# Optimization experiments

Hardware: AMD Instinct MI355X
Metric: run time of the kernel (lower is better)

Reference implementation:

```python
import jax, jax.numpy as jnp
import numpy as np

B, C_IN, H, W = 2, 256, 48, 48
OC, G, KH, KW, PH, PW = 256, 4, 7, 7, 3, 3


def _patches(y, Hn, Wn):
    # y: (B, C, Hp, Wp) -> (B, C, KH, KW, Hn, Wn); stride=1, dilation=1
    return jnp.stack([
        jnp.stack([y[:, :, i:i + Hn, j:j + Wn] for j in range(KW)], axis=2)
        for i in range(KH)
    ], axis=2)


def setup_inputs() -> dict:
    key = jax.random.key(0)
    k1, k2, k3, k4 = jax.random.split(key, 4)
    fan_out = 3 * OC  # 1x1 conv, kaiming fan_out
    conv_w = jax.random.normal(k2, (3 * OC, C_IN), dtype=jnp.float32) * np.sqrt(2.0 / fan_out).astype(np.float32)
    return {
        "x": jax.random.normal(k1, (B, C_IN, H, W), dtype=jnp.float32),
        "conv_w": conv_w,
        "rpe_h": jax.random.normal(k3, (G, 1, KH, 1, (OC // G) // 2), dtype=jnp.float32),
        "rpe_w": jax.random.normal(k4, (G, 1, 1, KW, (OC // G) // 2), dtype=jnp.float32),
    }


def reference(x, conv_w, rpe_h, rpe_w):
    b, c, h, w = x.shape
    goc = OC // G
    c2 = goc // 2
    K = KH * KW
    center = (K - 1) // 2
    ci, cj = center // KW, center % KW

    # 1x1 conv to 3*OC channels, then zero-pad (equiv. to Conv2d(padding) + bias=False)
    y = jnp.einsum('bchw,oc->bohw', x, conv_w)
    y = jnp.pad(y, ((0, 0), (0, 0), (PH, PH), (PW, PW)))
    Hn = h + 2 * PH - (KH - 1)
    Wn = w + 2 * PW - (KW - 1)
    P = Hn * Wn

    q_full, k_full, v_full = jnp.split(y, 3, axis=1)

    # query: only the center element of each window is used
    query = q_full[:, :, ci:ci + Hn, cj:cj + Wn].reshape(b, G, goc, P)
    query = jnp.transpose(query, (0, 1, 3, 2))  # (B,G,P,goc)

    # key: full windows + relative position embeddings
    kp = _patches(k_full, Hn, Wn).reshape(b, G, goc, KH, KW, P)
    key = jnp.transpose(kp, (0, 1, 5, 3, 4, 2))  # (B,G,P,KH,KW,goc)
    key = jnp.concatenate((key[..., :c2] + rpe_h, key[..., c2:] + rpe_w), axis=1)  # (B,2G,P,KH,KW,c2)
    key = key.reshape(b, G, P, K, goc)  # row-major reshape matches torch

    vp = _patches(v_full, Hn, Wn).reshape(b, G, goc, K, P)
    value = jnp.transpose(vp, (0, 1, 4, 3, 2))  # (B,G,P,K,goc)

    att = jax.nn.softmax(jnp.einsum('bgpc,bgpkc->bgpk', query, key), axis=-1)
    out = jnp.einsum('bgpk,bgpkc->bgpc', att, value)  # (B,G,P,goc)
    out = jnp.transpose(out, (0, 1, 3, 2)).reshape(b, OC, Hn, Wn)
    return out
```

## Files before the change

kernel.cpp:

```cpp
#include <hip/hip_runtime.h>

#define BB   2
#define CIN  256
#define OC3  768
#define NG   4
#define GOC  64
#define C2   32
#define KK   49
#define PP   2304
#define HALF_P 1152

#define RS      56
#define BROWS   54
#define BSTRIDE (BROWS * RS * OC3)
#define IOFF    ((3 * RS + 3) * OC3)

#define Y2_BYTES  (BB * BROWS * RS * OC3 * 4)
#define XT_OFF    Y2_BYTES
#define WT_OFF    (XT_OFF + BB * PP * 512 * 2)

typedef __attribute__((ext_vector_type(8))) short bf16x8;
typedef __attribute__((ext_vector_type(4))) float f32x4;

static __device__ __forceinline__ unsigned short f2bf_rne(float x) {
    unsigned int u = __float_as_uint(x);
    unsigned int r = u + 0x7FFFu + ((u >> 16) & 1u);
    return (unsigned short)(r >> 16);
}
static __device__ __forceinline__ float bf2f(unsigned short h) {
    return __uint_as_float(((unsigned int)h) << 16);
}

static __device__ __forceinline__ void gll16(const short* g, short* l) {
    __builtin_amdgcn_global_load_lds(
        (const __attribute__((address_space(1))) unsigned int*)g,
        (__attribute__((address_space(3))) unsigned int*)l,
        16, 0, 0);
}

template <int C>
static __device__ __forceinline__ float dppf(float x) {
    return __int_as_float(__builtin_amdgcn_update_dpp(
        0, __float_as_int(x), C, 0xF, 0xF, true));
}
template <int D>
static __device__ __forceinline__ float xor_lane(float x) {
    if constexpr (D == 1)       return dppf<0xB1>(x);
    else if constexpr (D == 2)  return dppf<0x4E>(x);
    else if constexpr (D == 4)  return dppf<0x141>(dppf<0x4E>(dppf<0xB1>(x)));
    else if constexpr (D == 8)  return dppf<0x128>(x);
    else                        return __shfl_xor(x, D, 64);
}
template <int N> struct IC { static constexpr int value = N; };

#define ROW4  (RS * OC3 / 4)
#define REG1  (6 * ROW4)
#define COLS4 (OC3 / 4)

__global__ __launch_bounds__(256) void prep(
    float* __restrict__ Y2,
    const float* __restrict__ W, short* __restrict__ Wt,
    const float* __restrict__ X, short* __restrict__ Xt)
{
    __shared__ float tile[64][65];
    const int bid = blockIdx.x;
    const int t   = threadIdx.x;

    if (bid < 1080) {
        const int idx = (bid % 540) * 256 + t;
        const int b   = bid / 540;
        float4* Yb = (float4*)(Y2 + (size_t)b * BSTRIDE);
        const float4 z = make_float4(0.f, 0.f, 0.f, 0.f);
        if (idx < REG1) {
            int r6  = idx / ROW4;
            int rem = idx - r6 * ROW4;
            int r   = (r6 < 3) ? r6 : 48 + r6;
            Yb[r * ROW4 + rem] = z;
        } else {
            int i2  = idx - REG1;
            int r   = 3 + i2 / (8 * COLS4);
            int rem = i2 - (r - 3) * (8 * COLS4);
            int cg  = rem / COLS4;
            int c   = (cg < 3) ? cg : 48 + cg;
            int ch4 = rem - cg * COLS4;
            Yb[(r * RS + c) * COLS4 + ch4] = z;
        }
    } else if (bid < 1848) {
        int tt = (bid - 1080) * 256 + t;
        int o = tt >> 8, c = tt & 255;
        float v = W[tt];
        unsigned short hi = f2bf_rne(v);
        unsigned short lo = f2bf_rne(v - bf2f(hi));
        Wt[(size_t)o * 512 + c]       = (short)hi;
        Wt[(size_t)o * 512 + 256 + c] = (short)lo;
    } else {
        const int blk = bid - 1848;
        const int p0  = (blk % 36) * 64;
        const int c0  = ((blk / 36) & 3) * 64;
        const int b   = blk / 144;

        const float* Xb = X + (size_t)b * CIN * PP;
        #pragma unroll
        for (int r = 0; r < 16; ++r) {
            int idx = r * 256 + t;
            int c = idx >> 6, p = idx & 63;
            tile[c][p] = Xb[(size_t)(c0 + c) * PP + p0 + p];
        }
        __syncthreads();
        short* Xo = Xt + (size_t)b * PP * 512;
        #pragma unroll
        for (int r = 0; r < 16; ++r) {
            int idx = r * 256 + t;
            int p = idx >> 6, c = idx & 63;
            float v = tile[c][p];
            unsigned short hi = f2bf_rne(v);
            unsigned short lo = f2bf_rne(v - bf2f(hi));
            size_t base = (size_t)(p0 + p) * 512 + c0 + c;
            Xo[base]       = (short)hi;
            Xo[base + 256] = (short)lo;
        }
    }
}

__global__ __launch_bounds__(256, 4) void conv_mfma(
    const short* __restrict__ Wt,
    const short* __restrict__ Xt,
    float* __restrict__ Y2)
{
    __shared__ short As[64 * 32];
    __shared__ short Bs[64 * 32];

    const int tid = threadIdx.x;
    const int bn  = blockIdx.x;
    const int bm  = blockIdx.y;
    const int b   = blockIdx.z;
    const int om0 = bm * 64, pn0 = bn * 64;

    const int lane = tid & 63, w = tid >> 6;
    const int oq = (w & 1) * 32, pq = (w >> 1) * 32;
    const int ln15 = lane & 15, q = lane >> 4;

    const int R  = (w << 4) + (lane >> 2);
    const int sd = (lane & 3) ^ ((R >> 1) & 3);
    const short* gAq = Wt + (size_t)(om0 + R) * 512 + sd * 8;
    const short* gBq = Xt + (size_t)b * PP * 512 + (size_t)(pn0 + R) * 512 + sd * 8;
    short* ldsA = As + w * 512;
    short* ldsB = Bs + w * 512;

    const int swz = q ^ ((ln15 >> 1) & 3);

    f32x4 acc[2][2] = {};

    for (int k0 = 0; k0 < 768; k0 += 32) {
        const int wk = (k0 < 256) ? k0 : k0 - 256;
        const int xk = (k0 < 512) ? k0 : k0 - 512;
        __syncthreads();
        gll16(gAq + wk, ldsA);
        gll16(gBq + xk, ldsB);
        __syncthreads();

        bf16x8 af[2], bf[2];
        #pragma unroll
        for (int i = 0; i < 2; ++i) {
            af[i] = *(const bf16x8*)&As[(oq + i * 16 + ln15) * 32 + swz * 8];
            bf[i] = *(const bf16x8*)&Bs[(pq + i * 16 + ln15) * 32 + swz * 8];
        }
        #pragma unroll
        for (int i = 0; i < 2; ++i)
            #pragma unroll
            for (int j = 0; j < 2; ++j)
                acc[i][j] = __builtin_amdgcn_mfma_f32_16x16x32_bf16(
                    af[i], bf[j], acc[i][j], 0, 0, 0);
    }

    float* Yb = Y2 + (size_t)b * BSTRIDE + IOFF;
    #pragma unroll
    for (int i = 0; i < 2; ++i) {
        #pragma unroll
        for (int j = 0; j < 2; ++j) {
            int o = om0 + oq + i * 16 + q * 4;
            int p = pn0 + pq + j * 16 + ln15;
            int h = p / 48, ww = p - h * 48;
            *(f32x4*)&Yb[(size_t)(h * RS + ww) * OC3 + o] = acc[i][j];
        }
    }
}

struct TagH { static constexpr bool value = true;  };
struct TagW { static constexpr bool value = false; };

__global__ __launch_bounds__(256, 6) void attn_kernel(
    const float* __restrict__ Y2,
    const float* __restrict__ rpe_h,
    const float* __restrict__ rpe_w,
    float* __restrict__ out)
{
    __shared__ float xpose[4][65];

    const int tid  = threadIdx.x;
    const int lane = tid & 63;
    const int w    = tid >> 6;
    const int bx     = blockIdx.x;
    const int wblock = (bx & 7) * 576 + (bx >> 3);
    const int wid    = wblock * 4 + w;
    const int pq   = wid % PP;
    const int g    = (wid / PP) & (NG - 1);
    const int b    = wid / (PP * NG);
    const int ph   = pq / 48;
    const int pw   = pq - ph * 48;

    const float* Yb = Y2 + (size_t)b * BSTRIDE + IOFF;

    const float qv = Yb[(size_t)(ph * RS + pw) * OC3 + g * GOC + lane];

    const int t   = (pq >= HALF_P) ? 1 : 0;
    const int qpr = pq - t * HALF_P;
    const int p0  = 2 * qpr;
    const int ph0 = p0 / 48;
    const int pw0 = p0 - ph0 * 48;
    const int g2  = 2 * g + t;
    const bool use_h = (g2 < NG);
    const int  kch   = use_h ? (CIN + g2 * GOC) : (CIN + (g2 - NG) * GOC + C2);
    const float* rb  = use_h ? (rpe_h + g2 * 7 * C2) : (rpe_w + (g2 - NG) * 7 * C2);

    const int  c  = lane & 31;
    const bool hi = (lane >= 32);

    const float R0 = rb[0 * C2 + c], R1 = rb[1 * C2 + c], R2 = rb[2 * C2 + c],
                R3 = rb[3 * C2 + c], R4 = rb[4 * C2 + c], R5 = rb[5 * C2 + c],
                R6 = rb[6 * C2 + c];

    const float* kb = Yb + (size_t)(ph0 * RS + pw0) * OC3 + kch + c;

    auto rget = [&](int idx) -> float {
        return idx == 0 ? R0 : idx == 1 ? R1 : idx == 2 ? R2 :
               idx == 3 ? R3 : idx == 4 ? R4 : idx == 5 ? R5 : R6;
    };

    auto tree = [&](auto tag) -> float {
        constexpr bool UH = decltype(tag)::value;
        auto chunkprod = [&](int l) -> float {
            int m0 = 2 * l,     h10 = (m0 >= KK), k0 = m0 - KK * h10;
            int m1 = 2 * l + 1, h11 = (m1 >= KK), k1 = m1 - KK * h11;
            int i0 = k0 / 7, j0 = k0 % 7, i1 = k1 / 7, j1 = k1 % 7;
            int d0 = ((i0 - 3) * RS + (h10 + j0 - 3)) * OC3;
            int d1 = ((i1 - 3) * RS + (h11 + j1 - 3)) * OC3;
            float kv = kb[hi ? d1 : d0];
            float ra = UH ? rget(i0) : rget(j0);
            float rc = UH ? rget(i1) : rget(j1);
            kv += hi ? rc : ra;
            return qv * kv;
        };
        auto val = [&](int jj) -> float {
            if (2 * jj >= KK) return 0.f;
            float pa = chunkprod(2 * jj);
            float pb = (2 * jj + 1 < KK) ? chunkprod(2 * jj + 1) : 0.f;
            float u  = (lane & 1) ? pb : pa;
            float ww = (lane & 1) ? pa : pb;
            return u + xor_lane<1>(ww);
        };
        auto comb = [&](auto dc, float x, float y) -> float {
            constexpr int d = decltype(dc)::value;
            float u  = (lane & d) ? y : x;
            float ww = (lane & d) ? x : y;
            return u + xor_lane<d>(ww);
        };
        float acc32[2];
        #pragma unroll
        for (int a = 0; a < 2; ++a) {
            float acc16[2];
            #pragma unroll
            for (int bq = 0; bq < 2; ++bq) {
                float acc8[2];
                #pragma unroll
                for (int cq2 = 0; cq2 < 2; ++cq2) {
                    float acc4t[2];
                    #pragma unroll
                    for (int dq = 0; dq < 2; ++dq) {
                        float acc2[2];
                        #pragma unroll
                        for (int eq = 0; eq < 2; ++eq)
                            acc2[eq] = val(a * 16 + bq * 8 + cq2 * 4 + dq * 2 + eq);
                        acc4t[dq] = comb(IC<2>{}, acc2[0], acc2[1]);
                    }
                    acc8[cq2] = comb(IC<4>{}, acc4t[0], acc4t[1]);
                }
                acc16[bq] = comb(IC<8>{}, acc8[0], acc8[1]);
            }
            acc32[a] = comb(IC<16>{}, acc16[0], acc16[1]);
        }
        return comb(IC<32>{}, acc32[0], acc32[1]);
    };

    const float logit = use_h ? tree(TagH{}) : tree(TagW{});

    float mx = logit;
    mx = fmaxf(mx, xor_lane<1>(mx));
    mx = fmaxf(mx, xor_lane<2>(mx));
    mx = fmaxf(mx, xor_lane<4>(mx));
    mx = fmaxf(mx, xor_lane<8>(mx));
    mx = fmaxf(mx, xor_lane<16>(mx));
    mx = fmaxf(mx, xor_lane<32>(mx));
    float e = (lane < KK) ? __expf(logit - mx) : 0.f;
    float ssum = e;
    ssum += xor_lane<1>(ssum);
    ssum += xor_lane<2>(ssum);
    ssum += xor_lane<4>(ssum);
    ssum += xor_lane<8>(ssum);
    ssum += xor_lane<16>(ssum);
    ssum += xor_lane<32>(ssum);
    const float att = e / ssum;

    float acc = 0.f;
    const float* vb = Yb + (size_t)(ph * RS + pw) * OC3 + 2 * CIN + g * GOC + lane;
    #pragma unroll
    for (int k = 0; k < KK; ++k) {
        int i = k / 7, j = k % 7;
        int doff = ((i - 3) * RS + (j - 3)) * OC3;
        float ak = __uint_as_float(
            __builtin_amdgcn_readlane(__float_as_uint(att), k));
        acc = fmaf(ak, vb[doff], acc);
    }

    xpose[w][lane] = acc;
    __syncthreads();
    const int wid0 = wblock * 4;
    const int pq0  = wid0 % PP;
    const int g0   = (wid0 / PP) & (NG - 1);
    const int b0   = wid0 / (PP * NG);
    const int ch   = tid >> 2;
    const int w2   = tid & 3;
    out[((size_t)b0 * 256 + g0 * GOC + ch) * PP + pq0 + w2] = xpose[w2][ch];
}

extern "C" void kernel_launch(void* const* d_in, const int* in_sizes, int n_in,
                              void* d_out, int out_size, void* d_ws, size_t ws_size,
                              hipStream_t stream)
{
    const float* x  = (const float*)d_in[0];
    const float* w  = (const float*)d_in[1];
    const float* rh = (const float*)d_in[2];
    const float* rw = (const float*)d_in[3];

    float* Y2 = (float*)d_ws;
    short* Xt = (short*)((char*)d_ws + XT_OFF);
    short* Wt = (short*)((char*)d_ws + WT_OFF);

    prep<<<2136, 256, 0, stream>>>(Y2, w, Wt, x, Xt);
    conv_mfma<<<dim3(36, 12, BB), 256, 0, stream>>>(Wt, Xt, Y2);
    attn_kernel<<<(BB * NG * PP) / 4, 256, 0, stream>>>(Y2, rh, rw, (float*)d_out);
}
```

Baseline: 110.6 us.

## Double-buffer conv LDS loads and move Y2 border zeroing into conv kernel

The conv GEMM loop now uses two LDS buffers, so the global-to-LDS load for the next K step is issued before the current step's MFMAs, and one barrier per iteration is dropped. The zero-padding of the Y2 border is moved out of the prep kernel into extra blocks of the conv grid (bm >= 12). This shortens prep and lets the zeroing run alongside the GEMM blocks. LDS use per block doubles, which may affect occupancy, and the extra grid rows add some scheduling overhead.

```diff
diff --git a/kernel.cpp b/kernel.cpp
--- a/kernel.cpp
+++ b/kernel.cpp
@@ -58,7 +58,6 @@
 #define COLS4 (OC3 / 4)
 
 __global__ __launch_bounds__(256) void prep(
-    float* __restrict__ Y2,
     const float* __restrict__ W, short* __restrict__ Wt,
     const float* __restrict__ X, short* __restrict__ Xt)
 {
@@ -66,9 +65,58 @@
     const int bid = blockIdx.x;
     const int t   = threadIdx.x;
 
-    if (bid < 1080) {
-        const int idx = (bid % 540) * 256 + t;
-        const int b   = bid / 540;
+    if (bid < 768) {
+        int tt = bid * 256 + t;
+        int o = tt >> 8, c = tt & 255;
+        float v = W[tt];
+        unsigned short hi = f2bf_rne(v);
+        unsigned short lo = f2bf_rne(v - bf2f(hi));
+        Wt[(size_t)o * 512 + c]       = (short)hi;
+        Wt[(size_t)o * 512 + 256 + c] = (short)lo;
+    } else {
+        const int blk = bid - 768;
+        const int p0  = (blk % 36) * 64;
+        const int c0  = ((blk / 36) & 3) * 64;
+        const int b   = blk / 144;
+
+        const float* Xb = X + (size_t)b * CIN * PP;
+        #pragma unroll
+        for (int r = 0; r < 16; ++r) {
+            int idx = r * 256 + t;
+            int c = idx >> 6, p = idx & 63;
+            tile[c][p] = Xb[(size_t)(c0 + c) * PP + p0 + p];
+        }
+        __syncthreads();
+        short* Xo = Xt + (size_t)b * PP * 512;
+        #pragma unroll
+        for (int r = 0; r < 16; ++r) {
+            int idx = r * 256 + t;
+            int p = idx >> 6, c = idx & 63;
+            float v = tile[c][p];
+            unsigned short hi = f2bf_rne(v);
+            unsigned short lo = f2bf_rne(v - bf2f(hi));
+            size_t base = (size_t)(p0 + p) * 512 + c0 + c;
+            Xo[base]       = (short)hi;
+            Xo[base + 256] = (short)lo;
+        }
+    }
+}
+
+__global__ __launch_bounds__(256, 4) void conv_mfma(
+    const short* __restrict__ Wt,
+    const short* __restrict__ Xt,
+    float* __restrict__ Y2)
+{
+    __shared__ short As[2][64 * 32];
+    __shared__ short Bs[2][64 * 32];
+
+    const int tid = threadIdx.x;
+    const int bn  = blockIdx.x;
+    const int bm  = blockIdx.y;
+    const int b   = blockIdx.z;
+
+    if (bm >= 12) {
+        const int idx = ((bm - 12) * 36 + bn) * 256 + tid;
         float4* Yb = (float4*)(Y2 + (size_t)b * BSTRIDE);
         const float4 z = make_float4(0.f, 0.f, 0.f, 0.f);
         if (idx < REG1) {
@@ -85,55 +133,9 @@
             int ch4 = rem - cg * COLS4;
             Yb[(r * RS + c) * COLS4 + ch4] = z;
         }
-    } else if (bid < 1848) {
-        int tt = (bid - 1080) * 256 + t;
-        int o = tt >> 8, c = tt & 255;
-        float v = W[tt];
-        unsigned short hi = f2bf_rne(v);
-        unsigned short lo = f2bf_rne(v - bf2f(hi));
-        Wt[(size_t)o * 512 + c]       = (short)hi;
-        Wt[(size_t)o * 512 + 256 + c] = (short)lo;
-    } else {
-        const int blk = bid - 1848;
-        const int p0  = (blk % 36) * 64;
-        const int c0  = ((blk / 36) & 3) * 64;
-        const int b   = blk / 144;
-
-        const float* Xb = X + (size_t)b * CIN * PP;
-        #pragma unroll
-        for (int r = 0; r < 16; ++r) {
-            int idx = r * 256 + t;
-            int c = idx >> 6, p = idx & 63;
-            tile[c][p] = Xb[(size_t)(c0 + c) * PP + p0 + p];
-        }
-        __syncthreads();
-        short* Xo = Xt + (size_t)b * PP * 512;
-        #pragma unroll
-        for (int r = 0; r < 16; ++r) {
-            int idx = r * 256 + t;
-            int p = idx >> 6, c = idx & 63;
-            float v = tile[c][p];
-            unsigned short hi = f2bf_rne(v);
-            unsigned short lo = f2bf_rne(v - bf2f(hi));
-            size_t base = (size_t)(p0 + p) * 512 + c0 + c;
-            Xo[base]       = (short)hi;
-            Xo[base + 256] = (short)lo;
-        }
-    }
-}
-
-__global__ __launch_bounds__(256, 4) void conv_mfma(
-    const short* __restrict__ Wt,
-    const short* __restrict__ Xt,
-    float* __restrict__ Y2)
-{
-    __shared__ short As[64 * 32];
-    __shared__ short Bs[64 * 32];
-
-    const int tid = threadIdx.x;
-    const int bn  = blockIdx.x;
-    const int bm  = blockIdx.y;
-    const int b   = blockIdx.z;
+        return;
+    }
+
     const int om0 = bm * 64, pn0 = bn * 64;
 
     const int lane = tid & 63, w = tid >> 6;
@@ -144,33 +146,41 @@
     const int sd = (lane & 3) ^ ((R >> 1) & 3);
     const short* gAq = Wt + (size_t)(om0 + R) * 512 + sd * 8;
     const short* gBq = Xt + (size_t)b * PP * 512 + (size_t)(pn0 + R) * 512 + sd * 8;
-    short* ldsA = As + w * 512;
-    short* ldsB = Bs + w * 512;
 
     const int swz = q ^ ((ln15 >> 1) & 3);
 
     f32x4 acc[2][2] = {};
 
-    for (int k0 = 0; k0 < 768; k0 += 32) {
-        const int wk = (k0 < 256) ? k0 : k0 - 256;
-        const int xk = (k0 < 512) ? k0 : k0 - 512;
-        __syncthreads();
-        gll16(gAq + wk, ldsA);
-        gll16(gBq + xk, ldsB);
-        __syncthreads();
+    gll16(gAq + 0, &As[0][w * 512]);
+    gll16(gBq + 0, &Bs[0][w * 512]);
+    __syncthreads();
+
+    for (int t = 0; t < 24; ++t) {
+        const int cur = t & 1;
 
         bf16x8 af[2], bf[2];
         #pragma unroll
         for (int i = 0; i < 2; ++i) {
-            af[i] = *(const bf16x8*)&As[(oq + i * 16 + ln15) * 32 + swz * 8];
-            bf[i] = *(const bf16x8*)&Bs[(pq + i * 16 + ln15) * 32 + swz * 8];
-        }
+            af[i] = *(const bf16x8*)&As[cur][(oq + i * 16 + ln15) * 32 + swz * 8];
+            bf[i] = *(const bf16x8*)&Bs[cur][(pq + i * 16 + ln15) * 32 + swz * 8];
+        }
+
+        if (t < 23) {
+            const int k0 = 32 * (t + 1);
+            const int wk = (k0 < 256) ? k0 : k0 - 256;
+            const int xk = (k0 < 512) ? k0 : k0 - 512;
+            gll16(gAq + wk, &As[cur ^ 1][w * 512]);
+            gll16(gBq + xk, &Bs[cur ^ 1][w * 512]);
+        }
+
         #pragma unroll
         for (int i = 0; i < 2; ++i)
             #pragma unroll
             for (int j = 0; j < 2; ++j)
                 acc[i][j] = __builtin_amdgcn_mfma_f32_16x16x32_bf16(
                     af[i], bf[j], acc[i][j], 0, 0, 0);
+
+        if (t < 23) __syncthreads();
     }
 
     float* Yb = Y2 + (size_t)b * BSTRIDE + IOFF;
@@ -346,7 +356,7 @@
     short* Xt = (short*)((char*)d_ws + XT_OFF);
     short* Wt = (short*)((char*)d_ws + WT_OFF);
 
-    prep<<<2136, 256, 0, stream>>>(Y2, w, Wt, x, Xt);
-    conv_mfma<<<dim3(36, 12, BB), 256, 0, stream>>>(Wt, Xt, Y2);
+    prep<<<1056, 256, 0, stream>>>(w, Wt, x, Xt);
+    conv_mfma<<<dim3(36, 27, BB), 256, 0, stream>>>(Wt, Xt, Y2);
     attn_kernel<<<(BB * NG * PP) / 4, 256, 0, stream>>>(Y2, rh, rw, (float*)d_out);
 }
```

Result: no change. 109.4 us (-1.1%).
